# Performance work log

Measured on AMD Instinct MI355X. Metric: run time of the kernel, lower is better.

Reference implementation:

```python
import jax, jax.numpy as jnp
import numpy as np

B, N, D = 2, 2048, 1024
H, HD = 16, 64
SCALE = HD ** (-0.5)


def setup_inputs() -> dict:
    key = jax.random.key(0)
    k1, k2, k3, k4 = jax.random.split(key, 4)
    x = jax.random.normal(k1, (B, N, D), dtype=jnp.float32)
    mask = jax.random.randint(k2, (B, 1, N, N), 0, 2) == 1  # bool, True = masked out
    W_qkv = jax.random.normal(k3, (D, 3 * H * HD), dtype=jnp.float32) * (D ** -0.5)
    W_out = jax.random.normal(k4, (H * HD, D), dtype=jnp.float32) * ((H * HD) ** -0.5)
    b_out = jnp.zeros((D,), dtype=jnp.float32)
    return {"x": x, "mask": mask, "W_qkv": W_qkv, "W_out": W_out, "b_out": b_out}


def reference(x, mask, W_qkv, W_out, b_out):
    b, n, _ = x.shape
    qkv = x @ W_qkv                                  # [b, n, 3*h*hd]
    q, k, v = jnp.split(qkv, 3, axis=-1)
    split_heads = lambda t: t.reshape(b, n, H, HD).transpose(0, 2, 1, 3)  # b h n d
    q, k, v = split_heads(q), split_heads(k), split_heads(v)
    scores = jnp.einsum('bhid,bhjd->bhij', q, k) * SCALE
    scores = jnp.where(mask, jnp.finfo(scores.dtype).min, scores)
    attn = jax.nn.softmax(scores, axis=-1)           # dropout p=0 -> identity
    out = jnp.einsum('bhij,bhjd->bhid', attn, v)     # [b, h, n, hd]
    out = out.transpose(0, 2, 1, 3).reshape(b, n, H * HD)
    return out @ W_out + b_out
```

## Files before the change

kernel.cpp:

```cpp
#include <hip/hip_runtime.h>
#include <stdint.h>

typedef unsigned short u16;
typedef short short8 __attribute__((ext_vector_type(8)));
typedef float f32x4 __attribute__((ext_vector_type(4)));
typedef float f32x16 __attribute__((ext_vector_type(16)));
typedef unsigned int uint2v __attribute__((ext_vector_type(2)));

#define K2E 0.18033688011112042f

__device__ __forceinline__ u16 f2bf(float f) {
  union { float f; uint32_t u; } v;
  v.f = f;
  uint32_t u = v.u;
  u += 0x7FFFu + ((u >> 16) & 1u);
  return (u16)(u >> 16);
}

__device__ __forceinline__ uint32_t cvtpk(float lo, float hi) {
  uint32_t r;
  asm("v_cvt_pk_bf16_f32 %0, %1, %2" : "=v"(r) : "v"(lo), "v"(hi));
  return r;
}

__device__ __forceinline__ float exp2a(float x) {
  float r;
  asm("v_exp_f32 %0, %1" : "=v"(r) : "v"(x));
  return r;
}

__device__ __forceinline__ float mask_zero(float p, uint32_t zm, int oc) {
  int mext = __builtin_amdgcn_sbfe((int)zm, oc, 1);
  float r;
  asm("v_bfi_b32 %0, %1, 0, %2" : "=v"(r) : "v"(mext), "v"(p));
  return r;
}

__device__ __forceinline__ void gld_lds16(const u16* src, char* dst) {
  __builtin_amdgcn_global_load_lds((const __attribute__((address_space(1))) void*)src,
                                   (__attribute__((address_space(3))) void*)dst, 16, 0, 0);
}

__device__ __forceinline__ void pack_frags(const f32x16& v, short8& fa, short8& fb) {
  union U { uint32_t w[4]; short8 v8; };
  uint32_t X0 = cvtpk(v[0], v[1]),   X1 = cvtpk(v[2], v[3]);
  uint32_t Y0 = cvtpk(v[4], v[5]),   Y1 = cvtpk(v[6], v[7]);
  uint32_t X2 = cvtpk(v[8], v[9]),   X3 = cvtpk(v[10], v[11]);
  uint32_t Y2 = cvtpk(v[12], v[13]), Y3 = cvtpk(v[14], v[15]);
  uint2v r0 = __builtin_amdgcn_permlane32_swap(X0, Y0, false, false);
  uint2v r1 = __builtin_amdgcn_permlane32_swap(X1, Y1, false, false);
  uint2v r2 = __builtin_amdgcn_permlane32_swap(X2, Y2, false, false);
  uint2v r3 = __builtin_amdgcn_permlane32_swap(X3, Y3, false, false);
  U ua; ua.w[0] = r0.x; ua.w[1] = r1.x; ua.w[2] = r0.y; ua.w[3] = r1.y; fa = ua.v8;
  U ub; ub.w[0] = r2.x; ub.w[1] = r3.x; ub.w[2] = r2.y; ub.w[3] = r3.y; fb = ub.v8;
}


__global__ __launch_bounds__(256) void k_cvt_x(const float* __restrict__ x,
                                               u16* __restrict__ xb, int n4) {
  int g = blockIdx.x * 256 + threadIdx.x;
  if (g >= n4) return;
  float4 v = ((const float4*)x)[g];
  ushort4 o;
  o.x = f2bf(v.x); o.y = f2bf(v.y); o.z = f2bf(v.z); o.w = f2bf(v.w);
  ((ushort4*)xb)[g] = o;
}

__global__ __launch_bounds__(256) void k_transpose_bf(const float* __restrict__ src,
                                                      u16* __restrict__ dst, int R, int C) {
  __shared__ float t[32][33];
  int c0 = blockIdx.x * 32, r0 = blockIdx.y * 32;
  int tx = threadIdx.x, ty = threadIdx.y;
#pragma unroll
  for (int i = 0; i < 4; ++i)
    t[ty + 8 * i][tx] = src[(size_t)(r0 + ty + 8 * i) * C + c0 + tx];
  __syncthreads();
#pragma unroll
  for (int i = 0; i < 4; ++i)
    dst[(size_t)(c0 + ty + 8 * i) * R + r0 + tx] = f2bf(t[tx][ty + 8 * i]);
}

__global__ __launch_bounds__(256) void k_mask_pack(const int* __restrict__ m,
                                                   uint32_t* __restrict__ w, int n) {
  int g = blockIdx.x * 256 + threadIdx.x;
  if (g >= n) return;
  unsigned long long bal = __ballot(m[g] != 0);
  int lane = threadIdx.x & 63;
  if (lane == 0) w[g >> 5] = (uint32_t)bal;
  else if (lane == 32) w[g >> 5] = (uint32_t)(bal >> 32);
}


#define GS(U, BUF)                                                   \
  {                                                                  \
    char* dA_ = lds + (BUF) * 16384 + (w << 11);                     \
    const u16* a_ = As + ((U) << 5);                                 \
    const u16* b_ = Bs + ((U) << 5);                                 \
    gld_lds16(a_, dA_);                                              \
    gld_lds16(a_ + (K << 4), dA_ + 1024);                            \
    gld_lds16(b_, dA_ + 8192);                                       \
    gld_lds16(b_ + (K << 4), dA_ + 9216);                            \
  }

#define PH(U, BUF, DOSTAGE, VMS)                                                          \
  {                                                                                       \
    asm volatile("s_waitcnt vmcnt(" VMS ")" ::: "memory");                                \
    __builtin_amdgcn_sched_barrier(0);                                                    \
    __builtin_amdgcn_s_barrier();                                                         \
    __builtin_amdgcn_sched_barrier(0);                                                    \
    const char* rb_ = lds + (BUF) * 16384;                                                \
    short8 af[4], bfr[4];                                                                 \
    _Pragma("unroll")                                                                     \
    for (int mi = 0; mi < 4; ++mi) {                                                      \
      int row = wm * 64 + mi * 16 + lr;                                                   \
      af[mi] = *(const short8*)(rb_ + row * 64 + ((lg ^ ((row >> 1) & 3)) << 4));         \
    }                                                                                     \
    _Pragma("unroll")                                                                     \
    for (int ni = 0; ni < 4; ++ni) {                                                      \
      int row = wn * 64 + ni * 16 + lr;                                                   \
      bfr[ni] = *(const short8*)(rb_ + 8192 + row * 64 + ((lg ^ ((row >> 1) & 3)) << 4)); \
    }                                                                                     \
    asm volatile("s_waitcnt lgkmcnt(0)" ::: "memory");                                    \
    __builtin_amdgcn_sched_barrier(0);                                                    \
    __builtin_amdgcn_s_barrier();                                                         \
    __builtin_amdgcn_sched_barrier(0);                                                    \
    if (DOSTAGE) GS((U) + 3, BUF);                                                        \
    __builtin_amdgcn_s_setprio(1);                                                        \
    _Pragma("unroll")                                                                     \
    for (int mi = 0; mi < 4; ++mi)                                                        \
      _Pragma("unroll")                                                                   \
      for (int ni = 0; ni < 4; ++ni)                                                      \
        acc[mi][ni] =                                                                     \
            __builtin_amdgcn_mfma_f32_16x16x32_bf16(af[mi], bfr[ni], acc[mi][ni], 0, 0, 0); \
    __builtin_amdgcn_s_setprio(0);                                                        \
  }

__device__ __forceinline__ void gemm_core(const u16* __restrict__ A,
                                          const u16* __restrict__ Bt,
                                          int K, int m0, int n0,
                                          f32x4 (&acc)[4][4], char* lds) {
  const int t = threadIdx.x;
  const int l = t & 63;
  const int w = t >> 6;
  const int wm = w >> 1, wn = w & 1;
  const int lr = l & 15, lg = l >> 4;
  const int r0 = (w << 5) + (l >> 2);
  const int c = (l & 3) ^ ((r0 >> 1) & 3);
  const u16* As = A + (size_t)(m0 + r0) * K + c * 8;
  const u16* Bs = Bt + (size_t)(n0 + r0) * K + c * 8;

  GS(0, 0);
  GS(1, 1);
  GS(2, 2);

#pragma unroll 1
  for (int i = 0; i < 9; ++i) {
    const int u = 3 * i;
    PH(u + 0, 0, true, "8");
    PH(u + 1, 1, true, "8");
    PH(u + 2, 2, true, "8");
  }
  PH(27, 0, true, "8");
  PH(28, 1, true, "8");
  PH(29, 2, false, "8");
  PH(30, 0, false, "4");
  PH(31, 1, false, "0");
}

__global__ __launch_bounds__(256, 3) void k_gemm_qkv(const u16* __restrict__ xb,
                                                     const u16* __restrict__ wqT,
                                                     u16* __restrict__ Qb,
                                                     u16* __restrict__ Kb,
                                                     u16* __restrict__ VT) {
  __shared__ char lds[49152] __attribute__((aligned(128)));
  int n0 = blockIdx.x * 128, m0 = blockIdx.y * 128;
  f32x4 acc[4][4] = {};
  gemm_core(xb, wqT, 1024, m0, n0, acc, lds);
  const int l = threadIdx.x & 63, w = threadIdx.x >> 6;
  const int wm = w >> 1, wn = w & 1;
  const int lr = l & 15, lg = l >> 4;
#pragma unroll
  for (int mi = 0; mi < 4; ++mi)
#pragma unroll
    for (int ni = 0; ni < 4; ++ni)
#pragma unroll
      for (int r = 0; r < 4; ++r) {
        int m = m0 + wm * 64 + mi * 16 + lg * 4 + r;
        int n = n0 + wn * 64 + ni * 16 + lr;
        int b = m >> 11, seq = m & 2047;
        float av = acc[mi][ni][r];
        if (n < 1024) {
          Qb[((size_t)((b << 4) + (n >> 6)) * 2048 + seq) * 64 + (n & 63)] = f2bf(av * K2E);
        } else if (n < 2048) {
          int nn = n - 1024;
          Kb[((size_t)((b << 4) + (nn >> 6)) * 2048 + seq) * 64 + (nn & 63)] = f2bf(av);
        } else {
          int nn = n - 2048;
          VT[((size_t)((b << 4) + (nn >> 6)) * 64 + (nn & 63)) * 2048 + seq] = f2bf(av);
        }
      }
}

__global__ __launch_bounds__(256, 3) void k_gemm_out(const u16* __restrict__ ao,
                                                     const u16* __restrict__ woT,
                                                     const float* __restrict__ bias,
                                                     float* __restrict__ out) {
  __shared__ char lds[49152] __attribute__((aligned(128)));
  int n0 = blockIdx.x * 128, m0 = blockIdx.y * 128;
  f32x4 acc[4][4] = {};
  gemm_core(ao, woT, 1024, m0, n0, acc, lds);
  const int l = threadIdx.x & 63, w = threadIdx.x >> 6;
  const int wm = w >> 1, wn = w & 1;
  const int lr = l & 15, lg = l >> 4;
#pragma unroll
  for (int mi = 0; mi < 4; ++mi)
#pragma unroll
    for (int ni = 0; ni < 4; ++ni)
#pragma unroll
      for (int r = 0; r < 4; ++r) {
        int m = m0 + wm * 64 + mi * 16 + lg * 4 + r;
        int n = n0 + wn * 64 + ni * 16 + lr;
        out[(size_t)m * 1024 + n] = acc[mi][ni][r] + bias[n];
      }
}

__global__ __launch_bounds__(512, 4) void k_attn(const u16* __restrict__ Qg,
                                                 const u16* __restrict__ Kg,
                                                 const u16* __restrict__ Vg,
                                                 const uint32_t* __restrict__ maskw,
                                                 u16* __restrict__ AO) {
  __shared__ char lds[65536] __attribute__((aligned(128)));
  const int bid = blockIdx.x;
  const int qt = bid & 15;
  const int hd = (bid >> 4) & 15;
  const int b = bid >> 8;
  const int bh = (b << 4) + hd;
  const int tx = threadIdx.x, l = tx & 63, w = tx >> 6;
  const int wq = w & 3, kvh = w >> 2;
  const int l31 = l & 31, h = l >> 5;
  const int hx4 = (h ^ (l & 7)) << 4;
  const int sc8 = ((l & 7) ^ (l >> 3)) << 3;
  const int lr8 = l >> 3;

  const u16* Qp = Qg + (size_t)bh * 131072;
  const int q = qt * 128 + wq * 32 + l31;
  const int kv0 = kvh << 10;

  const u16* kg = Kg + (size_t)bh * 131072 + (size_t)(kv0 + 16 * wq + lr8) * 64 + sc8;
  const u16* vg = Vg + (size_t)bh * 131072 + (size_t)(16 * wq + lr8) * 2048 + kv0 + sc8;
  const uint2v* mp = (const uint2v*)(maskw + ((size_t)(b << 11) + q) * 64) + (kvh << 4);

  short8 qf[4];
#pragma unroll
  for (int s = 0; s < 4; ++s)
    qf[s] = *(const short8*)(Qp + (size_t)q * 64 + s * 16 + h * 8);

  const short8 ones8 = {0x3F80, 0x3F80, 0x3F80, 0x3F80, 0x3F80, 0x3F80, 0x3F80, 0x3F80};
  f32x16 Oa[2] = {};
  f32x16 acc_l = {};
  char* ldsH = lds + (kvh << 15);

#define STAGE(BSEL, TT)                                       \
  {                                                           \
    char* base_ = ldsH + (BSEL) * 16384 + (wq << 11);         \
    const u16* k_ = kg + ((size_t)(TT) << 12);                \
    const u16* v_ = vg + ((size_t)(TT) << 6);                 \
    gld_lds16(k_, base_);                                     \
    gld_lds16(k_ + 512, base_ + 1024);                        \
    gld_lds16(v_, base_ + 8192);                              \
    gld_lds16(v_ + 16384, base_ + 9216);                      \
  }

  STAGE(0, 0);

#pragma unroll 1
  for (int tt = 0; tt < 16; ++tt) {
    __syncthreads();
    if (tt + 1 < 16) STAGE((tt + 1) & 1, tt + 1);
    const uint2v mm = mp[tt];
    const char* kbase = ldsH + (tt & 1) * 16384 + l31 * 128;
    const char* vbase = kbase + 8192;

    f32x16 sa = {}, sb = {};
    __builtin_amdgcn_s_setprio(1);
#pragma unroll
    for (int s = 0; s < 4; ++s) {
      short8 k0 = *(const short8*)(kbase + ((s << 5) ^ hx4));
      short8 k1 = *(const short8*)(kbase + 4096 + ((s << 5) ^ hx4));
      sa = __builtin_amdgcn_mfma_f32_32x32x16_bf16(k0, qf[s], sa, 0, 0, 0);
      sb = __builtin_amdgcn_mfma_f32_32x32x16_bf16(k1, qf[s], sb, 0, 0, 0);
    }
    __builtin_amdgcn_s_setprio(0);

    const uint32_t zm0 = mm.x >> (4 * h);
    const uint32_t zm1 = mm.y >> (4 * h);
#pragma unroll
    for (int r = 0; r < 16; ++r) {
      const int oc = (r & 3) + 8 * (r >> 2);
      sa[r] = mask_zero(exp2a(sa[r]), zm0, oc);
      sb[r] = mask_zero(exp2a(sb[r]), zm1, oc);
    }

    short8 pf[4];
    pack_frags(sa, pf[0], pf[1]);
    pack_frags(sb, pf[2], pf[3]);

    __builtin_amdgcn_s_setprio(1);
#pragma unroll
    for (int cc = 0; cc < 4; ++cc) {
      short8 v0 = *(const short8*)(vbase + ((cc << 5) ^ hx4));
      short8 v1 = *(const short8*)(vbase + 4096 + ((cc << 5) ^ hx4));
      Oa[0] = __builtin_amdgcn_mfma_f32_32x32x16_bf16(v0, pf[cc], Oa[0], 0, 0, 0);
      Oa[1] = __builtin_amdgcn_mfma_f32_32x32x16_bf16(v1, pf[cc], Oa[1], 0, 0, 0);
      acc_l = __builtin_amdgcn_mfma_f32_32x32x16_bf16(ones8, pf[cc], acc_l, 0, 0, 0);
    }
    __builtin_amdgcn_s_setprio(0);
  }
#undef STAGE

  __syncthreads();
  float* cb = (float*)lds;
  if (kvh) {
#pragma unroll
    for (int r = 0; r < 32; ++r)
      cb[((wq << 5) + r) * 64 + l] = Oa[r >> 4][r & 15];
    cb[8192 + (wq << 6) + l] = acc_l[0];
  }
  __syncthreads();
  if (!kvh) {
#pragma unroll
    for (int r = 0; r < 32; ++r)
      Oa[r >> 4][r & 15] += cb[((wq << 5) + r) * 64 + l];
    float lt = acc_l[0] + cb[8192 + (wq << 6) + l];
    float inv = 1.0f / fmaxf(lt, 1e-30f);
    u16* orow = AO + ((size_t)(b << 11) + q) * 1024 + hd * 64 + h * 4;
#pragma unroll
    for (int dt = 0; dt < 2; ++dt)
#pragma unroll
      for (int rq = 0; rq < 4; ++rq) {
        uint32_t w0 = cvtpk(Oa[dt][4 * rq + 0] * inv, Oa[dt][4 * rq + 1] * inv);
        uint32_t w1 = cvtpk(Oa[dt][4 * rq + 2] * inv, Oa[dt][4 * rq + 3] * inv);
        *(uint32_t*)(orow + dt * 32 + rq * 8) = w0;
        *(uint32_t*)(orow + dt * 32 + rq * 8 + 2) = w1;
      }
  }
}


extern "C" void kernel_launch(void* const* d_in, const int* in_sizes, int n_in,
                              void* d_out, int out_size, void* d_ws, size_t ws_size,
                              hipStream_t stream) {
  const float* x = (const float*)d_in[0];
  const int* mask = (const int*)d_in[1];
  const float* Wqkv = (const float*)d_in[2];
  const float* Wout = (const float*)d_in[3];
  const float* bout = (const float*)d_in[4];
  float* out = (float*)d_out;
  char* ws = (char*)d_ws;
  const size_t MB = 1u << 20;
  if (ws_size < 49 * MB) return;

  u16* xb = (u16*)(ws);
  u16* wqT = (u16*)(ws + 8 * MB);
  u16* woT = (u16*)(ws + 14 * MB);
  uint32_t* mw = (uint32_t*)(ws + 16 * MB);
  u16* Qb = (u16*)(ws + 17 * MB);
  u16* Kb = (u16*)(ws + 25 * MB);
  u16* VT = (u16*)(ws + 33 * MB);
  u16* AO = (u16*)(ws + 41 * MB);

  k_cvt_x<<<4096, 256, 0, stream>>>(x, xb, 1048576);
  k_transpose_bf<<<dim3(96, 32), dim3(32, 8), 0, stream>>>(Wqkv, wqT, 1024, 3072);
  k_transpose_bf<<<dim3(32, 32), dim3(32, 8), 0, stream>>>(Wout, woT, 1024, 1024);
  k_mask_pack<<<32768, 256, 0, stream>>>(mask, mw, 8388608);
  k_gemm_qkv<<<dim3(24, 32), 256, 0, stream>>>(xb, wqT, Qb, Kb, VT);
  k_attn<<<512, 512, 0, stream>>>(Qb, Kb, VT, mw, AO);
  k_gemm_out<<<dim3(8, 32), 256, 0, stream>>>(AO, woT, bout, out);
}
```

Before: 136.5 us.

## Rewrite QKV projection GEMM as 256x256 tile, 8-wave, double-buffered kernel

Replaces the 128x128 QKV GEMM, which used 4 waves and a triple-buffered 32-wide K loop, with a dedicated 256x256-tile kernel. It uses 512 threads, a 64-wide K step and 128KB of double-buffered LDS. Each wave computes a 128x64 sub-tile in four quadrant phases and interleaves global-to-LDS loads between them. The goal is more data reuse per load and fewer LDS/global reads per MFMA. The cost is a grid of only 192 blocks, fewer than the number of CUs, plus higher register and LDS pressure that limits occupancy.

```diff
diff --git a/kernel.cpp b/kernel.cpp
--- a/kernel.cpp
+++ b/kernel.cpp
@@ -88,6 +88,148 @@
   int lane = threadIdx.x & 63;
   if (lane == 0) w[g >> 5] = (uint32_t)bal;
   else if (lane == 32) w[g >> 5] = (uint32_t)(bal >> 32);
+}
+
+
+#define GQ_STAGE_A(T1)                                             \
+  {                                                                \
+    const size_t k0_ = (size_t)(T1) << 6;                          \
+    char* bb_ = lds + (((T1) & 1) << 16) + (w << 10);              \
+    const u16* s_ = pA + w8K + k0_;                                \
+    gld_lds16(s_, bb_);                                            \
+    gld_lds16(s_ + 64 * (size_t)GQK, bb_ + 8192);                  \
+    gld_lds16(s_ + 128 * (size_t)GQK, bb_ + 16384);                \
+    gld_lds16(s_ + 192 * (size_t)GQK, bb_ + 24576);                \
+  }
+#define GQ_STAGE_B(T1)                                             \
+  {                                                                \
+    const size_t k0_ = (size_t)(T1) << 6;                          \
+    char* bb_ = lds + (((T1) & 1) << 16) + 32768 + (w << 10);      \
+    const u16* s_ = pB + w8K + k0_;                                \
+    gld_lds16(s_, bb_);                                            \
+    gld_lds16(s_ + 64 * (size_t)GQK, bb_ + 8192);                  \
+    gld_lds16(s_ + 128 * (size_t)GQK, bb_ + 16384);                \
+    gld_lds16(s_ + 192 * (size_t)GQK, bb_ + 24576);                \
+  }
+
+#define GQ_RD_AF(MQ)                                               \
+  _Pragma("unroll")                                                \
+  for (int j = 0; j < 4; ++j) {                                    \
+    const char* ra_ = aB + ((MQ) * 64 + j * 16 + lr) * 128;        \
+    af[j][0] = *(const short8*)(ra_ + cof0);                       \
+    af[j][1] = *(const short8*)(ra_ + cof1);                       \
+  }
+#define GQ_RD_BF(NH)                                               \
+  _Pragma("unroll")                                                \
+  for (int nn = 0; nn < 2; ++nn) {                                 \
+    const char* rb_ = bB + (wn1 * 64 + ((NH) * 2 + nn) * 16 + lr) * 128; \
+    bfr[nn][0] = *(const short8*)(rb_ + cof0);                     \
+    bfr[nn][1] = *(const short8*)(rb_ + cof1);                     \
+  }
+
+#define GQ_MFMA(MQ, NH)                                            \
+  __builtin_amdgcn_s_setprio(1);                                   \
+  _Pragma("unroll")                                                \
+  for (int j = 0; j < 4; ++j)                                      \
+    _Pragma("unroll")                                              \
+    for (int nn = 0; nn < 2; ++nn) {                               \
+      acc[(MQ) * 4 + j][(NH) * 2 + nn] = __builtin_amdgcn_mfma_f32_16x16x32_bf16( \
+          af[j][0], bfr[nn][0], acc[(MQ) * 4 + j][(NH) * 2 + nn], 0, 0, 0);        \
+      acc[(MQ) * 4 + j][(NH) * 2 + nn] = __builtin_amdgcn_mfma_f32_16x16x32_bf16( \
+          af[j][1], bfr[nn][1], acc[(MQ) * 4 + j][(NH) * 2 + nn], 0, 0, 0);        \
+    }                                                              \
+  __builtin_amdgcn_s_setprio(0);
+
+#define GQ_LGKM                                                     \
+  asm volatile("s_waitcnt lgkmcnt(0)" ::: "memory");                \
+  __builtin_amdgcn_sched_barrier(0);
+#define GQ_BAR __builtin_amdgcn_s_barrier();
+
+#define GQK 1024
+
+__global__ __launch_bounds__(512, 2) void k_gemm_qkv(const u16* __restrict__ A,
+                                                     const u16* __restrict__ Bt,
+                                                     u16* __restrict__ Qb,
+                                                     u16* __restrict__ Kb,
+                                                     u16* __restrict__ VT) {
+  __shared__ char lds[131072] __attribute__((aligned(128)));
+  const int n0 = blockIdx.x * 256, m0 = blockIdx.y * 256;
+  const int t = threadIdx.x;
+  const int l = t & 63, w = t >> 6;
+  const int wm = w >> 2, wn = w & 3;
+  const int wn1 = wn & 1;
+  const int lr = l & 15, lg = l >> 4;
+  const int swl = ((lr >> 2) & 1) << 1;
+  const int cof0 = ((lg ^ swl) << 4);
+  const int cof1 = cof0 + 64;
+
+  const int d3l = l >> 3;
+  const int cse = ((l & 7) ^ (((l >> 5) & 1) << 1)) << 3;
+  const u16* pA = A + (size_t)(m0 + d3l) * GQK + cse;
+  const u16* pB = Bt + (size_t)(n0 + d3l) * GQK + cse;
+  const size_t w8K = (size_t)(8 * w) * GQK;
+
+  f32x4 acc[8][4] = {};
+  short8 af[4][2], bfr[2][2];
+
+  GQ_STAGE_A(0);
+  GQ_STAGE_B(0);
+
+#pragma unroll 1
+  for (int tt = 0; tt < 16; ++tt) {
+    const char* aB = lds + ((tt & 1) << 16) + wm * 16384;
+    const char* bB = lds + ((tt & 1) << 16) + 32768 + (wn >> 1) * 16384;
+    if (tt < 15) {
+      GQ_STAGE_A(tt + 1);
+      asm volatile("s_waitcnt vmcnt(4)" ::: "memory");
+    } else {
+      asm volatile("s_waitcnt vmcnt(0)" ::: "memory");
+    }
+    __builtin_amdgcn_sched_barrier(0);
+    GQ_BAR
+    GQ_RD_AF(0)
+    GQ_RD_BF(0)
+    GQ_LGKM
+    GQ_MFMA(0, 0)
+    GQ_BAR
+    if (tt < 15) GQ_STAGE_B(tt + 1);
+    GQ_RD_AF(1)
+    GQ_BAR
+    GQ_LGKM
+    GQ_MFMA(1, 0)
+    GQ_BAR
+    GQ_RD_BF(1)
+    GQ_BAR
+    GQ_LGKM
+    GQ_MFMA(1, 1)
+    GQ_BAR
+    GQ_RD_AF(0)
+    GQ_BAR
+    GQ_LGKM
+    GQ_MFMA(0, 1)
+    GQ_BAR
+  }
+
+#pragma unroll
+  for (int mi = 0; mi < 8; ++mi)
+#pragma unroll
+    for (int ni = 0; ni < 4; ++ni)
+#pragma unroll
+      for (int r = 0; r < 4; ++r) {
+        int m = m0 + wm * 128 + mi * 16 + lg * 4 + r;
+        int n = n0 + wn * 64 + ni * 16 + lr;
+        int b = m >> 11, seq = m & 2047;
+        float av = acc[mi][ni][r];
+        if (n < 1024) {
+          Qb[((size_t)((b << 4) + (n >> 6)) * 2048 + seq) * 64 + (n & 63)] = f2bf(av * K2E);
+        } else if (n < 2048) {
+          int nn = n - 1024;
+          Kb[((size_t)((b << 4) + (nn >> 6)) * 2048 + seq) * 64 + (nn & 63)] = f2bf(av);
+        } else {
+          int nn = n - 2048;
+          VT[((size_t)((b << 4) + (nn >> 6)) * 64 + (nn & 63)) * 2048 + seq] = f2bf(av);
+        }
+      }
 }
 
 
@@ -122,7 +264,7 @@
     }                                                                                     \
     asm volatile("s_waitcnt lgkmcnt(0)" ::: "memory");                                    \
     __builtin_amdgcn_sched_barrier(0);                                                    \
-    __builtin_amdgcn_s_barrier();                                                         \
+    __builtin_amdgcn_s_barrier();                                                        \
     __builtin_amdgcn_sched_barrier(0);                                                    \
     if (DOSTAGE) GS((U) + 3, BUF);                                                        \
     __builtin_amdgcn_s_setprio(1);                                                        \
@@ -165,40 +307,6 @@
   PH(29, 2, false, "8");
   PH(30, 0, false, "4");
   PH(31, 1, false, "0");
-}
-
-__global__ __launch_bounds__(256, 3) void k_gemm_qkv(const u16* __restrict__ xb,
-                                                     const u16* __restrict__ wqT,
-                                                     u16* __restrict__ Qb,
-                                                     u16* __restrict__ Kb,
-                                                     u16* __restrict__ VT) {
-  __shared__ char lds[49152] __attribute__((aligned(128)));
-  int n0 = blockIdx.x * 128, m0 = blockIdx.y * 128;
-  f32x4 acc[4][4] = {};
-  gemm_core(xb, wqT, 1024, m0, n0, acc, lds);
-  const int l = threadIdx.x & 63, w = threadIdx.x >> 6;
-  const int wm = w >> 1, wn = w & 1;
-  const int lr = l & 15, lg = l >> 4;
-#pragma unroll
-  for (int mi = 0; mi < 4; ++mi)
-#pragma unroll
-    for (int ni = 0; ni < 4; ++ni)
-#pragma unroll
-      for (int r = 0; r < 4; ++r) {
-        int m = m0 + wm * 64 + mi * 16 + lg * 4 + r;
-        int n = n0 + wn * 64 + ni * 16 + lr;
-        int b = m >> 11, seq = m & 2047;
-        float av = acc[mi][ni][r];
-        if (n < 1024) {
-          Qb[((size_t)((b << 4) + (n >> 6)) * 2048 + seq) * 64 + (n & 63)] = f2bf(av * K2E);
-        } else if (n < 2048) {
-          int nn = n - 1024;
-          Kb[((size_t)((b << 4) + (nn >> 6)) * 2048 + seq) * 64 + (nn & 63)] = f2bf(av);
-        } else {
-          int nn = n - 2048;
-          VT[((size_t)((b << 4) + (nn >> 6)) * 64 + (nn & 63)) * 2048 + seq] = f2bf(av);
-        }
-      }
 }
 
 __global__ __launch_bounds__(256, 3) void k_gemm_out(const u16* __restrict__ ao,
@@ -373,7 +481,7 @@
   k_transpose_bf<<<dim3(96, 32), dim3(32, 8), 0, stream>>>(Wqkv, wqT, 1024, 3072);
   k_transpose_bf<<<dim3(32, 32), dim3(32, 8), 0, stream>>>(Wout, woT, 1024, 1024);
   k_mask_pack<<<32768, 256, 0, stream>>>(mask, mw, 8388608);
-  k_gemm_qkv<<<dim3(24, 32), 256, 0, stream>>>(xb, wqT, Qb, Kb, VT);
+  k_gemm_qkv<<<dim3(12, 16), 512, 0, stream>>>(xb, wqT, Qb, Kb, VT);
   k_attn<<<512, 512, 0, stream>>>(Qb, Kb, VT, mw, AO);
   k_gemm_out<<<dim3(8, 32), 256, 0, stream>>>(AO, woT, bout, out);
 }
```

Measured after the change: 161.3 us. 1.18x slower.
